# Performance work log

Measured on AMD Instinct MI355X. Metric: run time of the kernel, lower is better.

## Reference

```python
import jax, jax.numpy as jnp
import numpy as np

B, C, N = 8, 512, 2048
C8 = C // 8


def setup_inputs() -> dict:
    key = jax.random.key(0)
    ks = jax.random.split(key, 8)
    s = 1.0 / np.sqrt(C)
    return {
        "x": jax.random.normal(ks[0], (B, C, N, 1, 1), jnp.float32),
        "y": jax.random.normal(ks[1], (B, C, N, 1, 1), jnp.float32),
        "Wq": jax.random.normal(ks[2], (C8, C), jnp.float32) * s,
        "bq": jax.random.normal(ks[3], (C8,), jnp.float32) * s,
        "Wk": jax.random.normal(ks[4], (C8, C), jnp.float32) * s,
        "bk": jax.random.normal(ks[5], (C8,), jnp.float32) * s,
        "Wv": jax.random.normal(ks[6], (C, C), jnp.float32) * s,
        "bv": jax.random.normal(ks[7], (C,), jnp.float32) * s,
        "gamma": jnp.zeros((1,), jnp.float32),
    }


def reference(x, y, Wq, bq, Wk, bk, Wv, bv, gamma):
    xs = x[..., 0, 0]  # [B, C, N]
    ys = y[..., 0, 0]  # [B, C, N]
    # 1x1 Conv1d == channel-wise linear
    q = jnp.einsum('oc,bcn->bon', Wq, ys) + bq[None, :, None]  # [B, C8, N]
    k = jnp.einsum('oc,bcn->bon', Wk, xs) + bk[None, :, None]  # [B, C8, N]
    v = jnp.einsum('oc,bcn->bon', Wv, ys) + bv[None, :, None]  # [B, C, N]
    energy = jnp.einsum('bon,bom->bnm', q, k)  # [B, Ny, Nx], unscaled
    attention = jax.nn.softmax(energy, axis=-1)
    # out[b,c,n] = sum_m v[b,c,m] * attention[b,n,m]
    out = jnp.einsum('bcm,bnm->bcn', v, attention)
    out = gamma * out + xs
    return out[..., None, None], attention
```

## Files before the change

kernel.cpp:

```cpp
#include <hip/hip_runtime.h>

#define B_ 8
#define C_ 512
#define N_ 2048
#define C8_ 64

typedef short s16x8 __attribute__((ext_vector_type(8)));
typedef float f32x4 __attribute__((ext_vector_type(4)));

__device__ __forceinline__ ushort bf16_rne(float f) {
    unsigned u = __float_as_uint(f);
    u += 0x7FFFu + ((u >> 16) & 1u);
    return (ushort)(u >> 16);
}
__device__ __forceinline__ float bf16_to_f(ushort h) {
    return __uint_as_float((unsigned)h << 16);
}

__global__ __launch_bounds__(256) void wsplit_kernel(
    const float* __restrict__ Wq, const float* __restrict__ Wk,
    ushort* __restrict__ wqhi, ushort* __restrict__ wqlo,
    ushort* __restrict__ wkhi, ushort* __restrict__ wklo)
{
    int idx = blockIdx.x * 256 + threadIdx.x;
    if (idx >= 2 * C8_ * C_) return;
    bool isq = idx < C8_ * C_;
    int i = isq ? idx : idx - C8_ * C_;
    float f = isq ? Wq[i] : Wk[i];
    ushort h = bf16_rne(f);
    ushort l = bf16_rne(f - bf16_to_f(h));
    if (isq) { wqhi[i] = h; wqlo[i] = l; }
    else     { wkhi[i] = h; wklo[i] = l; }
}

__global__ __launch_bounds__(128) void qk_mfma_kernel(
    const ushort* __restrict__ wqhi, const ushort* __restrict__ wqlo,
    const float* __restrict__ bq,  const float* __restrict__ ysrc,
    const ushort* __restrict__ wkhi, const ushort* __restrict__ wklo,
    const float* __restrict__ bk,  const float* __restrict__ xsrc,
    ushort* __restrict__ qhi, ushort* __restrict__ qlo,
    ushort* __restrict__ khi, ushort* __restrict__ klo)
{
    const int bid = blockIdx.x;
    const int id  = bid & 511;
    const bool isq = bid < 512;
    const ushort* __restrict__ whi  = isq ? wqhi : wkhi;
    const ushort* __restrict__ wlo  = isq ? wqlo : wklo;
    const float*  __restrict__ bias = isq ? bq : bk;
    const float*  __restrict__ src  = isq ? ysrc : xsrc;
    ushort* __restrict__ hi = isq ? qhi : khi;
    ushort* __restrict__ lo = isq ? qlo : klo;

    const int b  = id & 7;
    const int n0 = (id >> 3) * 32;
    const int w  = threadIdx.x >> 6;
    const int l  = threadIdx.x & 63;
    const int lc = l & 15;
    const int lq = l >> 4;
    const int nb = n0 + 16 * w;

    const float* ycol = src + ((unsigned)b * C_ * N_ + nb + lc);

    f32x4 acc[4];
    #pragma unroll
    for (int ot = 0; ot < 4; ++ot) acc[ot] = (f32x4){0.f, 0.f, 0.f, 0.f};

    #pragma unroll 4
    for (int ks = 0; ks < 16; ++ks) {
        const int c0 = ks * 32 + 8 * lq;
        float f[8];
        #pragma unroll
        for (int j = 0; j < 8; ++j)
            f[j] = ycol[(unsigned)(c0 + j) * N_];
        ushort ah[8], al[8];
        #pragma unroll
        for (int j = 0; j < 8; ++j) {
            ah[j] = bf16_rne(f[j]);
            al[j] = bf16_rne(f[j] - bf16_to_f(ah[j]));
        }
        s16x8 ahi, alo;
        #pragma unroll
        for (int j = 0; j < 8; ++j) { ahi[j] = (short)ah[j]; alo[j] = (short)al[j]; }

        #pragma unroll
        for (int ot = 0; ot < 4; ++ot) {
            const unsigned boff = (unsigned)(ot * 16 + lc) * C_ + ks * 32 + 8 * lq;
            s16x8 bhi = *(const s16x8*)(whi + boff);
            s16x8 blo = *(const s16x8*)(wlo + boff);
            f32x4 c = acc[ot];
            c = __builtin_amdgcn_mfma_f32_16x16x32_bf16(ahi, bhi, c, 0, 0, 0);
            c = __builtin_amdgcn_mfma_f32_16x16x32_bf16(ahi, blo, c, 0, 0, 0);
            c = __builtin_amdgcn_mfma_f32_16x16x32_bf16(alo, bhi, c, 0, 0, 0);
            acc[ot] = c;
        }
    }

    #pragma unroll
    for (int ot = 0; ot < 4; ++ot) {
        const int o = ot * 16 + lc;
        const float bs = bias[o];
        #pragma unroll
        for (int i = 0; i < 4; ++i) {
            float v = acc[ot][i] + bs;
            ushort h = bf16_rne(v);
            ushort s = bf16_rne(v - bf16_to_f(h));
            unsigned addr = ((unsigned)b * N_ + nb + lq * 4 + i) * C8_ + o;
            hi[addr] = h;
            lo[addr] = s;
        }
    }
}

__global__ __launch_bounds__(512, 4) void attn_kernel(
    const ushort* __restrict__ qhi, const ushort* __restrict__ qlo,
    const ushort* __restrict__ khi, const ushort* __restrict__ klo,
    float* __restrict__ att,
    const float* __restrict__ x, const float* __restrict__ gamma,
    float* __restrict__ out)
{
    const int b  = blockIdx.x & 7;
    const int n0 = (blockIdx.x >> 3) * 16;
    const int t  = threadIdx.x;
    const int w  = t >> 6;
    const int l  = t & 63;
    const int lc = l & 15;
    const int lq = l >> 4;

    if (gamma[0] == 0.0f) {
        #pragma unroll
        for (int p = 0; p < 4; ++p) {
            const int c = p * 128 + (t >> 2);
            const int j = t & 3;
            const unsigned off = ((unsigned)b * C_ + c) * N_ + n0 + 4 * j;
            *(float4*)(out + off) = *(const float4*)(x + off);
        }
    }

    const unsigned abase = ((unsigned)b * N_ + n0 + lc) * C8_ + 8 * lq;
    const s16x8* qhp = (const s16x8*)(qhi + abase);
    const s16x8* qlp = (const s16x8*)(qlo + abase);
    s16x8 ah0 = qhp[0], ah1 = qhp[4];
    s16x8 al0 = qlp[0], al1 = qlp[4];

    __shared__ char ldsk[65536];

    f32x4 acc[16];
    #pragma unroll
    for (int i = 0; i < 16; ++i) acc[i] = (f32x4){0.f, 0.f, 0.f, 0.f};

    const unsigned kbase = (unsigned)b * N_ * C8_;

    for (int chunk = 0; chunk < 8; ++chunk) {
        const unsigned cb = kbase + (unsigned)chunk * 256 * C8_;
        {
            s16x8 vh[4];
            #pragma unroll
            for (int it = 0; it < 4; ++it)
                vh[it] = *(const s16x8*)(khi + cb + it * 4096 + t * 8);
            #pragma unroll
            for (int it = 0; it < 4; ++it) {
                const unsigned s = (unsigned)it * 8192 + t * 16;
                const unsigned a = s ^ (((s >> 7) & 7u) << 4);
                *(s16x8*)(ldsk + a) = vh[it];
            }
            s16x8 vl[4];
            #pragma unroll
            for (int it = 0; it < 4; ++it)
                vl[it] = *(const s16x8*)(klo + cb + it * 4096 + t * 8);
            #pragma unroll
            for (int it = 0; it < 4; ++it) {
                const unsigned s = (unsigned)it * 8192 + t * 16;
                const unsigned a = s ^ (((s >> 7) & 7u) << 4);
                *(s16x8*)(ldsk + 32768 + a) = vl[it];
            }
        }
        __syncthreads();

        #pragma unroll
        for (int tt = 0; tt < 2; ++tt) {
            const unsigned r = (unsigned)w * 32 + tt * 16 + lc;
            const unsigned swz = (r & 7u) << 4;
            const unsigned a0 = (r * 128 + lq * 16) ^ swz;
            const unsigned a1 = (r * 128 + lq * 16 + 64) ^ swz;
            s16x8 bh0 = *(const s16x8*)(ldsk + a0);
            s16x8 bh1 = *(const s16x8*)(ldsk + a1);
            s16x8 bl0 = *(const s16x8*)(ldsk + 32768 + a0);
            s16x8 bl1 = *(const s16x8*)(ldsk + 32768 + a1);
            f32x4 c = acc[chunk * 2 + tt];
            c = __builtin_amdgcn_mfma_f32_16x16x32_bf16(ah0, bh0, c, 0, 0, 0);
            c = __builtin_amdgcn_mfma_f32_16x16x32_bf16(ah1, bh1, c, 0, 0, 0);
            c = __builtin_amdgcn_mfma_f32_16x16x32_bf16(ah0, bl0, c, 0, 0, 0);
            c = __builtin_amdgcn_mfma_f32_16x16x32_bf16(ah1, bl1, c, 0, 0, 0);
            c = __builtin_amdgcn_mfma_f32_16x16x32_bf16(al0, bh0, c, 0, 0, 0);
            c = __builtin_amdgcn_mfma_f32_16x16x32_bf16(al1, bh1, c, 0, 0, 0);
            acc[chunk * 2 + tt] = c;
        }
        __syncthreads();
    }

    #pragma unroll
    for (int ti = 0; ti < 16; ++ti)
        #pragma unroll
        for (int i = 0; i < 4; ++i)
            acc[ti][i] = __expf(acc[ti][i]);

    float* redsum = (float*)ldsk;
    float ssum[4];
    #pragma unroll
    for (int i = 0; i < 4; ++i) {
        float s = 0.f;
        #pragma unroll
        for (int ti = 0; ti < 16; ++ti) s += acc[ti][i];
        #pragma unroll
        for (int off = 1; off < 16; off <<= 1)
            s += __shfl_xor(s, off, 64);
        ssum[i] = s;
    }
    if (lc == 0) {
        #pragma unroll
        for (int i = 0; i < 4; ++i) redsum[(lq * 4 + i) * 8 + w] = ssum[i];
    }
    __syncthreads();
    float inv[4];
    #pragma unroll
    for (int i = 0; i < 4; ++i) {
        float s = redsum[(lq * 4 + i) * 8 + 0];
        #pragma unroll
        for (int ww = 1; ww < 8; ++ww) s += redsum[(lq * 4 + i) * 8 + ww];
        inv[i] = 1.0f / s;
    }
    __syncthreads();

    float* smem = (float*)ldsk;
    #pragma unroll
    for (int h = 0; h < 2; ++h) {
        if ((lq >> 1) == h) {
            const int rbase = (lq & 1) * 4;
            #pragma unroll
            for (int ti = 0; ti < 16; ++ti) {
                const unsigned col = (unsigned)(ti >> 1) * 256 +
                                     (unsigned)w * 32 + (ti & 1) * 16 + lc;
                #pragma unroll
                for (int i = 0; i < 4; ++i)
                    smem[(rbase + i) * 2048 + col] = acc[ti][i] * inv[i];
            }
        }
        __syncthreads();
        const int r = t >> 6;
        const int f = t & 63;
        float4* dst = (float4*)(att + ((unsigned)b * N_ + n0 + 8 * h + r) * N_);
        const float4* srcp = (const float4*)(smem + r * 2048);
        #pragma unroll
        for (int j = 0; j < 8; ++j)
            dst[f + 64 * j] = srcp[f + 64 * j];
        if (h == 0) __syncthreads();
    }
}

__global__ __launch_bounds__(256) void v_kernel(
    const float* __restrict__ Wv, const float* __restrict__ bv,
    const float* __restrict__ y, const float* __restrict__ gamma,
    float* __restrict__ v)
{
    if (gamma[0] == 0.0f) return;
    const size_t total = (size_t)B_ * C_ * N_;
    for (size_t idx = (size_t)blockIdx.x * 256 + threadIdx.x; idx < total;
         idx += (size_t)gridDim.x * 256) {
        int n = (int)(idx % N_);
        int o = (int)((idx / N_) % C_);
        int b = (int)(idx / ((size_t)N_ * C_));
        float s = bv[o];
        for (int c = 0; c < C_; ++c)
            s += Wv[o * C_ + c] * y[((size_t)b * C_ + c) * N_ + n];
        v[idx] = s;
    }
}

__global__ __launch_bounds__(256) void out_kernel(
    const float* __restrict__ x, const float* __restrict__ gamma,
    const float* __restrict__ v, const float* __restrict__ att,
    float* __restrict__ out)
{
    const float g = gamma[0];
    if (g == 0.0f) return;
    const size_t nf4 = (size_t)B_ * C_ * N_ / 4;
    const float4* x4 = (const float4*)x;
    float4* o4 = (float4*)out;
    for (size_t i = (size_t)blockIdx.x * blockDim.x + threadIdx.x; i < nf4;
         i += (size_t)gridDim.x * blockDim.x) {
        float4 xv = x4[i];
        size_t base = i * 4;
        int n = (int)(base % N_);
        int cch = (int)((base / N_) % C_);
        int b = (int)(base / ((size_t)N_ * C_));
        const float* vp = v + ((size_t)b * C_ + cch) * N_;
        const float* a0 = att + ((size_t)b * N_ + n) * N_;
        float s0 = 0.f, s1 = 0.f, s2 = 0.f, s3 = 0.f;
        for (int m = 0; m < N_; ++m) {
            float vv = vp[m];
            s0 += vv * a0[m];
            s1 += vv * a0[(size_t)N_ + m];
            s2 += vv * a0[2 * (size_t)N_ + m];
            s3 += vv * a0[3 * (size_t)N_ + m];
        }
        o4[i] = make_float4(g * s0 + xv.x, g * s1 + xv.y, g * s2 + xv.z, g * s3 + xv.w);
    }
}

extern "C" void kernel_launch(void* const* d_in, const int* in_sizes, int n_in,
                              void* d_out, int out_size, void* d_ws, size_t ws_size,
                              hipStream_t stream)
{
    const float* x     = (const float*)d_in[0];
    const float* y     = (const float*)d_in[1];
    const float* Wq    = (const float*)d_in[2];
    const float* bq    = (const float*)d_in[3];
    const float* Wk    = (const float*)d_in[4];
    const float* bk    = (const float*)d_in[5];
    const float* Wv    = (const float*)d_in[6];
    const float* bv    = (const float*)d_in[7];
    const float* gamma = (const float*)d_in[8];

    float* out = (float*)d_out;
    float* att = (float*)d_out + (size_t)B_ * C_ * N_;

    char* ws = (char*)d_ws;
    ushort* wqhi = (ushort*)(ws);
    ushort* wqlo = (ushort*)(ws + (64u << 10));
    ushort* wkhi = (ushort*)(ws + (128u << 10));
    ushort* wklo = (ushort*)(ws + (192u << 10));
    ushort* qhi  = (ushort*)(ws + (1u << 20));
    ushort* qlo  = (ushort*)(ws + (3u << 20));
    ushort* khi  = (ushort*)(ws + (5u << 20));
    ushort* klo  = (ushort*)(ws + (7u << 20));
    float*  vbuf = (float*) (ws + (10u << 20));

    wsplit_kernel<<<(2 * C8_ * C_ + 255) / 256, 256, 0, stream>>>(
        Wq, Wk, wqhi, wqlo, wkhi, wklo);

    qk_mfma_kernel<<<1024, 128, 0, stream>>>(
        wqhi, wqlo, bq, y, wkhi, wklo, bk, x, qhi, qlo, khi, klo);

    attn_kernel<<<1024, 512, 0, stream>>>(qhi, qlo, khi, klo, att, x, gamma, out);

    v_kernel<<<1024, 256, 0, stream>>>(Wv, bv, y, gamma, vbuf);
    out_kernel<<<2048, 256, 0, stream>>>(x, gamma, vbuf, att, out);
}
```

Baseline: 300.6 us.

## Double-buffer K chunks in LDS via direct global-to-LDS async loads

```diff
diff --git a/kernel.cpp b/kernel.cpp
--- a/kernel.cpp
+++ b/kernel.cpp
@@ -15,6 +15,13 @@
 }
 __device__ __forceinline__ float bf16_to_f(ushort h) {
     return __uint_as_float((unsigned)h << 16);
+}
+
+__device__ __forceinline__ void gll16(const void* g, void* l) {
+    __builtin_amdgcn_global_load_lds(
+        (const __attribute__((address_space(1))) void*)g,
+        (__attribute__((address_space(3))) void*)l,
+        16, 0, 0);
 }
 
 __global__ __launch_bounds__(256) void wsplit_kernel(
@@ -126,6 +133,35 @@
     const int lc = l & 15;
     const int lq = l >> 4;
 
+    __shared__ char ldsk[65536];
+
+    const unsigned kbase = (unsigned)b * N_ * C8_;
+
+    auto stage = [&](int chunk) {
+        const unsigned cb = kbase + (unsigned)chunk * 128 * C8_;
+        const unsigned bufoff = (unsigned)(chunk & 1) * 32768;
+        #pragma unroll
+        for (int it = 0; it < 2; ++it) {
+            const unsigned ub = (unsigned)it * 8192 + (unsigned)w * 1024;
+            const unsigned u  = ub + (unsigned)l * 16;
+            const unsigned srcb = u ^ (((u >> 7) & 7u) << 4);
+            gll16((const char*)(khi + cb) + srcb, ldsk + bufoff + ub);
+            gll16((const char*)(klo + cb) + srcb, ldsk + bufoff + 16384 + ub);
+        }
+    };
+
+    const unsigned abase = ((unsigned)b * N_ + n0 + lc) * C8_ + 8 * lq;
+    const s16x8* qhp = (const s16x8*)(qhi + abase);
+    const s16x8* qlp = (const s16x8*)(qlo + abase);
+    s16x8 ah0 = qhp[0], ah1 = qhp[4];
+    s16x8 al0 = qlp[0], al1 = qlp[4];
+
+    f32x4 acc[16];
+    #pragma unroll
+    for (int i = 0; i < 16; ++i) acc[i] = (f32x4){0.f, 0.f, 0.f, 0.f};
+
+    stage(0);
+
     if (gamma[0] == 0.0f) {
         #pragma unroll
         for (int p = 0; p < 4; ++p) {
@@ -135,66 +171,28 @@
             *(float4*)(out + off) = *(const float4*)(x + off);
         }
     }
-
-    const unsigned abase = ((unsigned)b * N_ + n0 + lc) * C8_ + 8 * lq;
-    const s16x8* qhp = (const s16x8*)(qhi + abase);
-    const s16x8* qlp = (const s16x8*)(qlo + abase);
-    s16x8 ah0 = qhp[0], ah1 = qhp[4];
-    s16x8 al0 = qlp[0], al1 = qlp[4];
-
-    __shared__ char ldsk[65536];
-
-    f32x4 acc[16];
-    #pragma unroll
-    for (int i = 0; i < 16; ++i) acc[i] = (f32x4){0.f, 0.f, 0.f, 0.f};
-
-    const unsigned kbase = (unsigned)b * N_ * C8_;
-
-    for (int chunk = 0; chunk < 8; ++chunk) {
-        const unsigned cb = kbase + (unsigned)chunk * 256 * C8_;
-        {
-            s16x8 vh[4];
-            #pragma unroll
-            for (int it = 0; it < 4; ++it)
-                vh[it] = *(const s16x8*)(khi + cb + it * 4096 + t * 8);
-            #pragma unroll
-            for (int it = 0; it < 4; ++it) {
-                const unsigned s = (unsigned)it * 8192 + t * 16;
-                const unsigned a = s ^ (((s >> 7) & 7u) << 4);
-                *(s16x8*)(ldsk + a) = vh[it];
-            }
-            s16x8 vl[4];
-            #pragma unroll
-            for (int it = 0; it < 4; ++it)
-                vl[it] = *(const s16x8*)(klo + cb + it * 4096 + t * 8);
-            #pragma unroll
-            for (int it = 0; it < 4; ++it) {
-                const unsigned s = (unsigned)it * 8192 + t * 16;
-                const unsigned a = s ^ (((s >> 7) & 7u) << 4);
-                *(s16x8*)(ldsk + 32768 + a) = vl[it];
-            }
-        }
-        __syncthreads();
-
-        #pragma unroll
-        for (int tt = 0; tt < 2; ++tt) {
-            const unsigned r = (unsigned)w * 32 + tt * 16 + lc;
-            const unsigned swz = (r & 7u) << 4;
-            const unsigned a0 = (r * 128 + lq * 16) ^ swz;
-            const unsigned a1 = (r * 128 + lq * 16 + 64) ^ swz;
-            s16x8 bh0 = *(const s16x8*)(ldsk + a0);
-            s16x8 bh1 = *(const s16x8*)(ldsk + a1);
-            s16x8 bl0 = *(const s16x8*)(ldsk + 32768 + a0);
-            s16x8 bl1 = *(const s16x8*)(ldsk + 32768 + a1);
-            f32x4 c = acc[chunk * 2 + tt];
-            c = __builtin_amdgcn_mfma_f32_16x16x32_bf16(ah0, bh0, c, 0, 0, 0);
-            c = __builtin_amdgcn_mfma_f32_16x16x32_bf16(ah1, bh1, c, 0, 0, 0);
-            c = __builtin_amdgcn_mfma_f32_16x16x32_bf16(ah0, bl0, c, 0, 0, 0);
-            c = __builtin_amdgcn_mfma_f32_16x16x32_bf16(ah1, bl1, c, 0, 0, 0);
-            c = __builtin_amdgcn_mfma_f32_16x16x32_bf16(al0, bh0, c, 0, 0, 0);
-            c = __builtin_amdgcn_mfma_f32_16x16x32_bf16(al1, bh1, c, 0, 0, 0);
-            acc[chunk * 2 + tt] = c;
-        }
+    __syncthreads();
+
+    #pragma unroll
+    for (int c = 0; c < 16; ++c) {
+        if (c < 15) stage(c + 1);
+        const unsigned base = (unsigned)(c & 1) * 32768;
+        const unsigned r = (unsigned)w * 16 + lc;
+        const unsigned swz = (r & 7u) << 4;
+        const unsigned a0 = base + ((r * 128 + lq * 16) ^ swz);
+        const unsigned a1 = base + ((r * 128 + 64 + lq * 16) ^ swz);
+        s16x8 bh0 = *(const s16x8*)(ldsk + a0);
+        s16x8 bh1 = *(const s16x8*)(ldsk + a1);
+        s16x8 bl0 = *(const s16x8*)(ldsk + 16384 + a0);
+        s16x8 bl1 = *(const s16x8*)(ldsk + 16384 + a1);
+        f32x4 cc = acc[c];
+        cc = __builtin_amdgcn_mfma_f32_16x16x32_bf16(ah0, bh0, cc, 0, 0, 0);
+        cc = __builtin_amdgcn_mfma_f32_16x16x32_bf16(ah1, bh1, cc, 0, 0, 0);
+        cc = __builtin_amdgcn_mfma_f32_16x16x32_bf16(ah0, bl0, cc, 0, 0, 0);
+        cc = __builtin_amdgcn_mfma_f32_16x16x32_bf16(ah1, bl1, cc, 0, 0, 0);
+        cc = __builtin_amdgcn_mfma_f32_16x16x32_bf16(al0, bh0, cc, 0, 0, 0);
+        cc = __builtin_amdgcn_mfma_f32_16x16x32_bf16(al1, bh1, cc, 0, 0, 0);
+        acc[c] = cc;
         __syncthreads();
     }
 
@@ -238,8 +236,7 @@
             const int rbase = (lq & 1) * 4;
             #pragma unroll
             for (int ti = 0; ti < 16; ++ti) {
-                const unsigned col = (unsigned)(ti >> 1) * 256 +
-                                     (unsigned)w * 32 + (ti & 1) * 16 + lc;
+                const unsigned col = (unsigned)ti * 128 + (unsigned)w * 16 + lc;
                 #pragma unroll
                 for (int i = 0; i < 4; ++i)
                     smem[(rbase + i) * 2048 + col] = acc[ti][i] * inv[i];
```

Result: faster. 289.3 us (-3.8%).
